# Performance work log

Hardware: AMD Instinct MI355X
Metric: run time of the kernel (lower is better)

Reference implementation:

```python
import jax, jax.numpy as jnp
import numpy as np

N = 62      # EEG channels / graph nodes
F = 5       # features per node (frequency bands)
H = 64      # num_hiddens
C = 3       # num_classes
K = 2       # SGC propagation steps
B = 32768   # batch size
BN_EPS = 1e-5
NORM_EPS = 1e-10


def setup_inputs() -> dict:
    key = jax.random.key(0)
    ks = jax.random.split(key, 8)
    n_tril = N * (N + 1) // 2  # 1953 lower-tri (incl diag) learnable edge weights
    return {
        "X": jax.random.normal(ks[0], (B, N, F), dtype=jnp.float32),
        "edge_w_tril": jax.random.normal(ks[1], (n_tril,), dtype=jnp.float32),
        "bn_gamma": jnp.ones((F,), dtype=jnp.float32),
        "bn_beta": jnp.zeros((F,), dtype=jnp.float32),
        "lin_W": jax.random.normal(ks[2], (F, H), dtype=jnp.float32) * 0.1,
        "lin_b": jax.random.normal(ks[3], (H,), dtype=jnp.float32) * 0.1,
        "fc1_W": jax.random.normal(ks[4], (N * H, 64), dtype=jnp.float32) * 0.02,
        "fc1_b": jax.random.normal(ks[5], (64,), dtype=jnp.float32) * 0.02,
        "fc2_W": jax.random.normal(ks[6], (64, C), dtype=jnp.float32) * 0.1,
        "fc2_b": jax.random.normal(ks[7], (C,), dtype=jnp.float32) * 0.1,
    }


def _propagation_matrix(edge_w_tril):
    # Rebuild symmetric learnable adjacency from lower-tri params
    xs, ys = jnp.tril_indices(N)
    W = jnp.zeros((N, N), dtype=edge_w_tril.dtype).at[xs, ys].set(edge_w_tril)
    W = W + W.T - jnp.diag(jnp.diag(W))
    # normalize_A: relu + D^{-1/2} A D^{-1/2}
    A = jax.nn.relu(W)
    d = jnp.sum(A, axis=1)
    dinv = 1.0 / jnp.sqrt(d + NORM_EPS)
    L = dinv[:, None] * A * dinv[None, :]
    # NewSGConv.norm: add self-loops (weight 1), deg = row-sum of |w|,
    # norm_ij = deg_i^{-1/2} w_ij deg_j^{-1/2}. Dense form since edge list is all-pairs.
    deg = jnp.sum(jnp.abs(L), axis=1) + 1.0  # +1 from self-loop
    dis = 1.0 / jnp.sqrt(deg)                 # deg >= 1, no inf
    S = dis[:, None] * (L + jnp.eye(N, dtype=L.dtype)) * dis[None, :]
    return S


def _forward(X, edge_w_tril, bn_gamma, bn_beta, lin_W, lin_b, fc1_W, fc1_b, fc2_W, fc2_b):
    # BatchNorm1d over feature dim (training mode: batch stats over (B, N)), biased var
    mean = jnp.mean(X, axis=(0, 1))
    var = jnp.mean(jnp.square(X - mean), axis=(0, 1))
    x = (X - mean) / jnp.sqrt(var + BN_EPS) * bn_gamma + bn_beta  # (B, N, F)

    S = _propagation_matrix(edge_w_tril)  # (N, N)
    # K steps of SGC propagation: x <- S x (gather-scale-scatter == dense matmul here)
    for _ in range(K):
        x = jnp.einsum('ij,bjf->bif', S, x)
    x = jnp.einsum('bnf,fh->bnh', x, lin_W) + lin_b  # SGConv linear, (B, N, H)

    x = x.reshape(x.shape[0], -1)                    # (B, N*H)
    x = jax.nn.relu(x @ fc1_W + fc1_b)
    return x @ fc2_W + fc2_b                         # (B, C) logits


def reference(X, edge_w_tril, bn_gamma, bn_beta, lin_W, lin_b, fc1_W, fc1_b, fc2_W, fc2_b):
    return _forward(X, edge_w_tril, bn_gamma, bn_beta, lin_W, lin_b,
                    fc1_W, fc1_b, fc2_W, fc2_b)
```

## Files before the change

kernel.cpp:

```cpp
#include <hip/hip_runtime.h>
#include <math.h>


#define STATS_BLOCKS 496
#define BN_COUNT 2031616.0f

__global__ __launch_bounds__(256) void k_stats(const float* __restrict__ X,
                                               float* __restrict__ part)
{
    int tid = blockIdx.x * 256 + threadIdx.x;
    const float4* Xv = reinterpret_cast<const float4*>(X) + (size_t)tid * 20;
    float s[5] = {0.f,0.f,0.f,0.f,0.f};
    float q[5] = {0.f,0.f,0.f,0.f,0.f};
#pragma unroll
    for (int v = 0; v < 20; ++v) {
        float4 x = Xv[v];
        s[(4*v+0)%5] += x.x; q[(4*v+0)%5] += x.x*x.x;
        s[(4*v+1)%5] += x.y; q[(4*v+1)%5] += x.y*x.y;
        s[(4*v+2)%5] += x.z; q[(4*v+2)%5] += x.z*x.z;
        s[(4*v+3)%5] += x.w; q[(4*v+3)%5] += x.w*x.w;
    }
#pragma unroll
    for (int k = 0; k < 5; ++k) {
#pragma unroll
        for (int m = 32; m >= 1; m >>= 1) {
            s[k] += __shfl_xor(s[k], m);
            q[k] += __shfl_xor(q[k], m);
        }
    }
    __shared__ float red[4][10];
    int lane = threadIdx.x & 63, w = threadIdx.x >> 6;
    if (lane == 0) {
#pragma unroll
        for (int k = 0; k < 5; ++k) { red[w][k] = s[k]; red[w][5+k] = q[k]; }
    }
    __syncthreads();
    if (threadIdx.x < 10)
        part[blockIdx.x*10 + threadIdx.x] =
            red[0][threadIdx.x] + red[1][threadIdx.x] +
            red[2][threadIdx.x] + red[3][threadIdx.x];
}

__global__ __launch_bounds__(256) void k_setup(
    const float* __restrict__ part, const float* __restrict__ edge,
    const float* __restrict__ gamma, const float* __restrict__ beta,
    const float* __restrict__ linW, const float* __restrict__ linb,
    const float* __restrict__ fc1W, const float* __restrict__ fc1b,
    float* __restrict__ Meff, float* __restrict__ constv)
{
    const int o = blockIdx.x;
    const int t = threadIdx.x;
    __shared__ float Amat[62*62];
    __shared__ float S2m[62*62];
    __shared__ float colo[3968];
    __shared__ float Tm[310];
    __shared__ float lw[320];
    __shared__ float dv[62];
    __shared__ float dis[62];
    __shared__ float scale[5], shift[5];
    __shared__ float redbuf[256];

    {
        float st[10];
#pragma unroll
        for (int k = 0; k < 10; ++k) st[k] = 0.f;
        for (int b = t; b < STATS_BLOCKS; b += 256) {
#pragma unroll
            for (int k = 0; k < 10; ++k) st[k] += part[b*10 + k];
        }
#pragma unroll
        for (int k = 0; k < 10; ++k) {
#pragma unroll
            for (int m = 32; m >= 1; m >>= 1) st[k] += __shfl_xor(st[k], m);
        }
        int lane = t & 63, w = t >> 6;
        if (lane == 0)
            for (int k = 0; k < 10; ++k) redbuf[w*10 + k] = st[k];
    }
    for (int e = t; e < 3844; e += 256) {
        int i = e / 62, j = e % 62;
        int idx = (i >= j) ? (i*(i+1)/2 + j) : (j*(j+1)/2 + i);
        Amat[e] = fmaxf(edge[idx], 0.f);
    }
    for (int i = t; i < 3968; i += 256) colo[i] = fc1W[(size_t)i*64 + o];
    for (int i = t; i < 320;  i += 256) lw[i] = linW[i];
    __syncthreads();

    if (t < 10)
        redbuf[64 + t] = redbuf[t] + redbuf[10+t] + redbuf[20+t] + redbuf[30+t];
    __syncthreads();
    if (t < 5) {
        float mean = redbuf[64 + t] * (1.0f / BN_COUNT);
        float var  = redbuf[69 + t] * (1.0f / BN_COUNT) - mean*mean;
        float inv  = 1.0f / sqrtf(var + 1e-5f);
        scale[t] = gamma[t] * inv;
        shift[t] = beta[t] - mean * gamma[t] * inv;
    }
    if (t < 62) {
        float sum = 0.f;
        for (int j = 0; j < 62; ++j) sum += Amat[t*62 + j];
        dv[t] = 1.0f / sqrtf(sum + 1e-10f);
    }
    __syncthreads();
    for (int e = t; e < 3844; e += 256) {
        int i = e / 62, j = e % 62;
        Amat[e] *= dv[i] * dv[j];
    }
    __syncthreads();
    if (t < 62) {
        float deg = 1.0f;
        for (int j = 0; j < 62; ++j) deg += fabsf(Amat[t*62 + j]);
        dis[t] = 1.0f / sqrtf(deg);
    }
    __syncthreads();
    for (int e = t; e < 3844; e += 256) {
        int i = e / 62, j = e % 62;
        float v = Amat[e] + ((i == j) ? 1.0f : 0.0f);
        Amat[e] = dis[i] * v * dis[j];
    }
    __syncthreads();
    for (int e = t; e < 3844; e += 256) {
        int i = e / 62, j = e % 62;
        float sum = 0.f;
        for (int k = 0; k < 62; ++k) sum += Amat[i*62 + k] * Amat[k*62 + j];
        S2m[e] = sum;
    }
    __syncthreads();
    for (int p = t; p < 310; p += 256) {
        int n = p / 5, f = p % 5;
        float sum = 0.f;
        for (int h = 0; h < 64; ++h) sum += lw[f*64 + h] * colo[n*64 + h];
        Tm[p] = sum;
    }
    __syncthreads();
    float cpart = 0.f;
    for (int p = t; p < 310; p += 256) {
        int j = p / 5, f = p % 5;
        float m = 0.f;
        for (int n = 0; n < 62; ++n) m += S2m[n*62 + j] * Tm[n*5 + f];
        Meff[(size_t)p*64 + o] = scale[f] * m;
        cpart += shift[f] * m;
    }
    for (int nh = t; nh < 3968; nh += 256)
        cpart += linb[nh & 63] * colo[nh];
    __syncthreads();
    redbuf[t] = cpart;
    __syncthreads();
    for (int sft = 128; sft > 0; sft >>= 1) {
        if (t < sft) redbuf[t] += redbuf[t + sft];
        __syncthreads();
    }
    if (t == 0) constv[o] = redbuf[0] + fc1b[o];
}

__global__ __launch_bounds__(256) void k_gemm(
    const float* __restrict__ X, const float* __restrict__ Meff,
    const float* __restrict__ constv, const float* __restrict__ fc2W,
    const float* __restrict__ fc2b, float* __restrict__ out)
{
    __shared__ float Ms[62*64];
    __shared__ float Xs[62*68];
    __shared__ float cst[64];
    __shared__ float f2[192];
    const int t = threadIdx.x;
    const int row0 = blockIdx.x * 64;
    const int tc = t & 15;
    const int tr = t >> 4;
    float acc[4][4];
#pragma unroll
    for (int a = 0; a < 4; ++a)
#pragma unroll
        for (int b = 0; b < 4; ++b) acc[a][b] = 0.f;

    if (t < 64)       cst[t]      = constv[t];
    else if (t < 256) { if (t - 64 < 192) f2[t - 64] = fc2W[t - 64]; }

    const int r  = t >> 2;
    const int qt = t & 3;
    const int u0 = qt * 16;
    const int ulim = (qt == 3) ? 14 : 16;

    for (int c = 0; c < 5; ++c) {
        __syncthreads();
        const float4* msrc = reinterpret_cast<const float4*>(Meff + c*3968);
        float4* mdst = reinterpret_cast<float4*>(Ms);
        for (int i = t; i < 992; i += 256) mdst[i] = msrc[i];
        const float* xrow = X + (size_t)(row0 + r)*310 + c*62 + u0;
#pragma unroll
        for (int uu = 0; uu < 16; uu += 2) {
            if (uu < ulim) {
                float2 v = *reinterpret_cast<const float2*>(xrow + uu);
                Xs[(u0 + uu    )*68 + r] = v.x;
                Xs[(u0 + uu + 1)*68 + r] = v.y;
            }
        }
        __syncthreads();
#pragma unroll 2
        for (int u = 0; u < 62; ++u) {
            float4 xv = *reinterpret_cast<const float4*>(Xs + u*68 + tr*4);
            float4 mv = *reinterpret_cast<const float4*>(Ms + u*64 + tc*4);
            acc[0][0] += xv.x*mv.x; acc[0][1] += xv.x*mv.y; acc[0][2] += xv.x*mv.z; acc[0][3] += xv.x*mv.w;
            acc[1][0] += xv.y*mv.x; acc[1][1] += xv.y*mv.y; acc[1][2] += xv.y*mv.z; acc[1][3] += xv.y*mv.w;
            acc[2][0] += xv.z*mv.x; acc[2][1] += xv.z*mv.y; acc[2][2] += xv.z*mv.z; acc[2][3] += xv.z*mv.w;
            acc[3][0] += xv.w*mv.x; acc[3][1] += xv.w*mv.y; acc[3][2] += xv.w*mv.z; acc[3][3] += xv.w*mv.w;
        }
    }

    float prt[4][3];
#pragma unroll
    for (int qq = 0; qq < 4; ++qq) { prt[qq][0] = prt[qq][1] = prt[qq][2] = 0.f; }
#pragma unroll
    for (int qq = 0; qq < 4; ++qq) {
#pragma unroll
        for (int p = 0; p < 4; ++p) {
            int col = tc*4 + p;
            float z = fmaxf(acc[qq][p] + cst[col], 0.f);
            prt[qq][0] += z * f2[col*3 + 0];
            prt[qq][1] += z * f2[col*3 + 1];
            prt[qq][2] += z * f2[col*3 + 2];
        }
    }
#pragma unroll
    for (int m = 1; m < 16; m <<= 1) {
#pragma unroll
        for (int qq = 0; qq < 4; ++qq) {
            prt[qq][0] += __shfl_xor(prt[qq][0], m);
            prt[qq][1] += __shfl_xor(prt[qq][1], m);
            prt[qq][2] += __shfl_xor(prt[qq][2], m);
        }
    }
    if (tc == 0) {
        float b0 = fc2b[0], b1 = fc2b[1], b2 = fc2b[2];
#pragma unroll
        for (int qq = 0; qq < 4; ++qq) {
            size_t rw = (size_t)(row0 + tr*4 + qq) * 3;
            out[rw + 0] = prt[qq][0] + b0;
            out[rw + 1] = prt[qq][1] + b1;
            out[rw + 2] = prt[qq][2] + b2;
        }
    }
}

extern "C" void kernel_launch(void* const* d_in, const int* in_sizes, int n_in,
                              void* d_out, int out_size, void* d_ws, size_t ws_size,
                              hipStream_t stream)
{
    const float* X     = (const float*)d_in[0];
    const float* edge  = (const float*)d_in[1];
    const float* gamma = (const float*)d_in[2];
    const float* beta  = (const float*)d_in[3];
    const float* linW  = (const float*)d_in[4];
    const float* linb  = (const float*)d_in[5];
    const float* fc1W  = (const float*)d_in[6];
    const float* fc1b  = (const float*)d_in[7];
    const float* fc2W  = (const float*)d_in[8];
    const float* fc2b  = (const float*)d_in[9];
    float* out = (float*)d_out;
    float* ws  = (float*)d_ws;

    float* part   = ws;
    float* Meff   = ws + 4960;
    float* constv = ws + 24800;

    hipLaunchKernelGGL(k_stats, dim3(496), dim3(256), 0, stream, X, part);
    hipLaunchKernelGGL(k_setup, dim3(64), dim3(256), 0, stream,
                       part, edge, gamma, beta, linW, linb, fc1W, fc1b, Meff, constv);
    hipLaunchKernelGGL(k_gemm, dim3(512), dim3(256), 0, stream,
                       X, Meff, constv, fc2W, fc2b, out);
}
```

Before: 158.4 us.

## Pre-transpose X in a separate kernel and run register-streamed GEMM without LDS

Adds a k_tp kernel that transposes X into a column-major workspace copy (XT). Its extra block computes the squared propagation matrix once instead of once per setup block. The GEMM now streams XT and Meff straight from global memory into registers with double buffering, dropping LDS staging and the per-chunk barriers, and sets launch bounds for two blocks per unit. This spends an extra full read and write of X (about 40 MB) to get coalesced vector loads and higher occupancy in the GEMM.

```diff
diff --git a/kernel.cpp b/kernel.cpp
--- a/kernel.cpp
+++ b/kernel.cpp
@@ -41,8 +41,82 @@
             red[2][threadIdx.x] + red[3][threadIdx.x];
 }
 
+__global__ __launch_bounds__(256) void k_tp(const float* __restrict__ X,
+                                            const float* __restrict__ edge,
+                                            float* __restrict__ XT,
+                                            float* __restrict__ S2g)
+{
+    __shared__ __align__(16) float lds[4160];
+    const int t = threadIdx.x;
+    if (blockIdx.x < 512) {
+        const int row0 = blockIdx.x * 64;
+        for (int cc = 0; cc < 5; ++cc) {
+            const int c0 = cc * 62;
+            if (cc) __syncthreads();
+            for (int i = t; i < 3968; i += 256) {
+                int r = i / 62, u = i - r * 62;
+                lds[u * 65 + r] = X[(size_t)(row0 + r) * 310 + c0 + u];
+            }
+            __syncthreads();
+            for (int j = t; j < 3968; j += 256) {
+                int u = j >> 6, r = j & 63;
+                XT[(size_t)(c0 + u) * 32768 + row0 + r] = lds[u * 65 + r];
+            }
+        }
+    } else {
+        float* Sm  = lds;
+        float* dv  = lds + 3968;
+        float* dis = lds + 4032;
+        for (int e = t; e < 3968; e += 256) {
+            int i = e >> 6, j = e & 63;
+            float v = 0.f;
+            if (j < 62) {
+                int idx = (i >= j) ? (i*(i+1)/2 + j) : (j*(j+1)/2 + i);
+                v = fmaxf(edge[idx], 0.f);
+            }
+            Sm[e] = v;
+        }
+        __syncthreads();
+        if (t < 62) {
+            float s = 0.f;
+            for (int j = 0; j < 64; ++j) s += Sm[t*64 + j];
+            dv[t] = 1.0f / sqrtf(s + 1e-10f);
+        }
+        __syncthreads();
+        for (int e = t; e < 3968; e += 256) {
+            int i = e >> 6, j = e & 63;
+            if (j < 62) Sm[e] *= dv[i] * dv[j];
+        }
+        __syncthreads();
+        if (t < 62) {
+            float dg = 1.0f;
+            for (int j = 0; j < 64; ++j) dg += fabsf(Sm[t*64 + j]);
+            dis[t] = 1.0f / sqrtf(dg);
+        }
+        __syncthreads();
+        for (int e = t; e < 3968; e += 256) {
+            int i = e >> 6, j = e & 63;
+            if (j < 62) {
+                float v = Sm[e] + ((i == j) ? 1.0f : 0.0f);
+                Sm[e] = dis[i] * v * dis[j];
+            }
+        }
+        __syncthreads();
+        for (int g = t; g < 992; g += 256) {
+            int i = g >> 4, j0 = (g & 15) << 2;
+            float4 acc = {0.f, 0.f, 0.f, 0.f};
+            for (int k = 0; k < 62; ++k) {
+                float s = Sm[i*64 + k];
+                float4 b = *reinterpret_cast<const float4*>(&Sm[k*64 + j0]);
+                acc.x += s*b.x; acc.y += s*b.y; acc.z += s*b.z; acc.w += s*b.w;
+            }
+            *reinterpret_cast<float4*>(&S2g[i*64 + j0]) = acc;
+        }
+    }
+}
+
 __global__ __launch_bounds__(256) void k_setup(
-    const float* __restrict__ part, const float* __restrict__ edge,
+    const float* __restrict__ part, const float* __restrict__ S2g,
     const float* __restrict__ gamma, const float* __restrict__ beta,
     const float* __restrict__ linW, const float* __restrict__ linb,
     const float* __restrict__ fc1W, const float* __restrict__ fc1b,
@@ -50,13 +124,10 @@
 {
     const int o = blockIdx.x;
     const int t = threadIdx.x;
-    __shared__ float Amat[62*62];
-    __shared__ float S2m[62*62];
+    __shared__ float S2m[3968];
     __shared__ float colo[3968];
     __shared__ float Tm[310];
     __shared__ float lw[320];
-    __shared__ float dv[62];
-    __shared__ float dis[62];
     __shared__ float scale[5], shift[5];
     __shared__ float redbuf[256];
 
@@ -77,13 +148,11 @@
         if (lane == 0)
             for (int k = 0; k < 10; ++k) redbuf[w*10 + k] = st[k];
     }
-    for (int e = t; e < 3844; e += 256) {
-        int i = e / 62, j = e % 62;
-        int idx = (i >= j) ? (i*(i+1)/2 + j) : (j*(j+1)/2 + i);
-        Amat[e] = fmaxf(edge[idx], 0.f);
-    }
-    for (int i = t; i < 3968; i += 256) colo[i] = fc1W[(size_t)i*64 + o];
-    for (int i = t; i < 320;  i += 256) lw[i] = linW[i];
+    for (int i = t; i < 3968; i += 256) {
+        S2m[i]  = S2g[i];
+        colo[i] = fc1W[(size_t)i*64 + o];
+    }
+    for (int i = t; i < 320; i += 256) lw[i] = linW[i];
     __syncthreads();
 
     if (t < 10)
@@ -96,38 +165,8 @@
         scale[t] = gamma[t] * inv;
         shift[t] = beta[t] - mean * gamma[t] * inv;
     }
-    if (t < 62) {
-        float sum = 0.f;
-        for (int j = 0; j < 62; ++j) sum += Amat[t*62 + j];
-        dv[t] = 1.0f / sqrtf(sum + 1e-10f);
-    }
-    __syncthreads();
-    for (int e = t; e < 3844; e += 256) {
-        int i = e / 62, j = e % 62;
-        Amat[e] *= dv[i] * dv[j];
-    }
-    __syncthreads();
-    if (t < 62) {
-        float deg = 1.0f;
-        for (int j = 0; j < 62; ++j) deg += fabsf(Amat[t*62 + j]);
-        dis[t] = 1.0f / sqrtf(deg);
-    }
-    __syncthreads();
-    for (int e = t; e < 3844; e += 256) {
-        int i = e / 62, j = e % 62;
-        float v = Amat[e] + ((i == j) ? 1.0f : 0.0f);
-        Amat[e] = dis[i] * v * dis[j];
-    }
-    __syncthreads();
-    for (int e = t; e < 3844; e += 256) {
-        int i = e / 62, j = e % 62;
-        float sum = 0.f;
-        for (int k = 0; k < 62; ++k) sum += Amat[i*62 + k] * Amat[k*62 + j];
-        S2m[e] = sum;
-    }
-    __syncthreads();
     for (int p = t; p < 310; p += 256) {
-        int n = p / 5, f = p % 5;
+        int n = p / 5, f = p - n*5;
         float sum = 0.f;
         for (int h = 0; h < 64; ++h) sum += lw[f*64 + h] * colo[n*64 + h];
         Tm[p] = sum;
@@ -135,9 +174,9 @@
     __syncthreads();
     float cpart = 0.f;
     for (int p = t; p < 310; p += 256) {
-        int j = p / 5, f = p % 5;
+        int j = p / 5, f = p - j*5;
         float m = 0.f;
-        for (int n = 0; n < 62; ++n) m += S2m[n*62 + j] * Tm[n*5 + f];
+        for (int n = 0; n < 62; ++n) m += S2m[n*64 + j] * Tm[n*5 + f];
         Meff[(size_t)p*64 + o] = scale[f] * m;
         cpart += shift[f] * m;
     }
@@ -153,90 +192,97 @@
     if (t == 0) constv[o] = redbuf[0] + fc1b[o];
 }
 
-__global__ __launch_bounds__(256) void k_gemm(
-    const float* __restrict__ X, const float* __restrict__ Meff,
+struct Ch { float4 xa[5]; float4 m[5]; };
+
+__device__ __forceinline__ void ldch(Ch& c, const float* px, const float* pm, int u0) {
+#pragma unroll
+    for (int k = 0; k < 5; ++k) {
+        c.xa[k] = *reinterpret_cast<const float4*>(px + (size_t)(u0 + k) * 32768);
+        c.m[k]  = *reinterpret_cast<const float4*>(pm + (u0 + k) * 64);
+    }
+}
+
+__device__ __forceinline__ void fmach(float acc[4][4], const Ch& c) {
+#pragma unroll
+    for (int k = 0; k < 5; ++k) {
+        float4 x = c.xa[k], m = c.m[k];
+        acc[0][0] += x.x*m.x; acc[0][1] += x.x*m.y; acc[0][2] += x.x*m.z; acc[0][3] += x.x*m.w;
+        acc[1][0] += x.y*m.x; acc[1][1] += x.y*m.y; acc[1][2] += x.y*m.z; acc[1][3] += x.y*m.w;
+        acc[2][0] += x.z*m.x; acc[2][1] += x.z*m.y; acc[2][2] += x.z*m.z; acc[2][3] += x.z*m.w;
+        acc[3][0] += x.w*m.x; acc[3][1] += x.w*m.y; acc[3][2] += x.w*m.z; acc[3][3] += x.w*m.w;
+    }
+}
+
+__global__ __launch_bounds__(256, 2) void k_gemm(
+    const float* __restrict__ XT, const float* __restrict__ Meff,
     const float* __restrict__ constv, const float* __restrict__ fc2W,
     const float* __restrict__ fc2b, float* __restrict__ out)
 {
-    __shared__ float Ms[62*64];
-    __shared__ float Xs[62*68];
-    __shared__ float cst[64];
-    __shared__ float f2[192];
     const int t = threadIdx.x;
-    const int row0 = blockIdx.x * 64;
     const int tc = t & 15;
     const int tr = t >> 4;
+    const int row0 = blockIdx.x * 64;
+    const float* px = XT + row0 + tr * 4;
+    const float* pm = Meff + tc * 4;
     float acc[4][4];
 #pragma unroll
     for (int a = 0; a < 4; ++a)
 #pragma unroll
         for (int b = 0; b < 4; ++b) acc[a][b] = 0.f;
 
-    if (t < 64)       cst[t]      = constv[t];
-    else if (t < 256) { if (t - 64 < 192) f2[t - 64] = fc2W[t - 64]; }
-
-    const int r  = t >> 2;
-    const int qt = t & 3;
-    const int u0 = qt * 16;
-    const int ulim = (qt == 3) ? 14 : 16;
-
-    for (int c = 0; c < 5; ++c) {
-        __syncthreads();
-        const float4* msrc = reinterpret_cast<const float4*>(Meff + c*3968);
-        float4* mdst = reinterpret_cast<float4*>(Ms);
-        for (int i = t; i < 992; i += 256) mdst[i] = msrc[i];
-        const float* xrow = X + (size_t)(row0 + r)*310 + c*62 + u0;
-#pragma unroll
-        for (int uu = 0; uu < 16; uu += 2) {
-            if (uu < ulim) {
-                float2 v = *reinterpret_cast<const float2*>(xrow + uu);
-                Xs[(u0 + uu    )*68 + r] = v.x;
-                Xs[(u0 + uu + 1)*68 + r] = v.y;
-            }
-        }
-        __syncthreads();
-#pragma unroll 2
-        for (int u = 0; u < 62; ++u) {
-            float4 xv = *reinterpret_cast<const float4*>(Xs + u*68 + tr*4);
-            float4 mv = *reinterpret_cast<const float4*>(Ms + u*64 + tc*4);
-            acc[0][0] += xv.x*mv.x; acc[0][1] += xv.x*mv.y; acc[0][2] += xv.x*mv.z; acc[0][3] += xv.x*mv.w;
-            acc[1][0] += xv.y*mv.x; acc[1][1] += xv.y*mv.y; acc[1][2] += xv.y*mv.z; acc[1][3] += xv.y*mv.w;
-            acc[2][0] += xv.z*mv.x; acc[2][1] += xv.z*mv.y; acc[2][2] += xv.z*mv.z; acc[2][3] += xv.z*mv.w;
-            acc[3][0] += xv.w*mv.x; acc[3][1] += xv.w*mv.y; acc[3][2] += xv.w*mv.z; acc[3][3] += xv.w*mv.w;
-        }
-    }
-
+    Ch A, B;
+    ldch(A, px, pm, 0);
+#pragma unroll 1
+    for (int i = 0; i < 30; ++i) {
+        ldch(B, px, pm, 5);
+        fmach(acc, A);
+        px += 10 * 32768; pm += 10 * 64;
+        ldch(A, px, pm, 0);
+        fmach(acc, B);
+    }
+    ldch(B, px, pm, 5);
+    fmach(acc, A);
+    fmach(acc, B);
+
+    float cst[4], f2r[4][3];
+#pragma unroll
+    for (int j = 0; j < 4; ++j) {
+        int col = tc*4 + j;
+        cst[j]    = constv[col];
+        f2r[j][0] = fc2W[col*3 + 0];
+        f2r[j][1] = fc2W[col*3 + 1];
+        f2r[j][2] = fc2W[col*3 + 2];
+    }
     float prt[4][3];
 #pragma unroll
-    for (int qq = 0; qq < 4; ++qq) { prt[qq][0] = prt[qq][1] = prt[qq][2] = 0.f; }
-#pragma unroll
-    for (int qq = 0; qq < 4; ++qq) {
-#pragma unroll
-        for (int p = 0; p < 4; ++p) {
-            int col = tc*4 + p;
-            float z = fmaxf(acc[qq][p] + cst[col], 0.f);
-            prt[qq][0] += z * f2[col*3 + 0];
-            prt[qq][1] += z * f2[col*3 + 1];
-            prt[qq][2] += z * f2[col*3 + 2];
+    for (int q = 0; q < 4; ++q) { prt[q][0] = prt[q][1] = prt[q][2] = 0.f; }
+#pragma unroll
+    for (int q = 0; q < 4; ++q) {
+#pragma unroll
+        for (int j = 0; j < 4; ++j) {
+            float z = fmaxf(acc[q][j] + cst[j], 0.f);
+            prt[q][0] += z * f2r[j][0];
+            prt[q][1] += z * f2r[j][1];
+            prt[q][2] += z * f2r[j][2];
         }
     }
 #pragma unroll
     for (int m = 1; m < 16; m <<= 1) {
 #pragma unroll
-        for (int qq = 0; qq < 4; ++qq) {
-            prt[qq][0] += __shfl_xor(prt[qq][0], m);
-            prt[qq][1] += __shfl_xor(prt[qq][1], m);
-            prt[qq][2] += __shfl_xor(prt[qq][2], m);
+        for (int q = 0; q < 4; ++q) {
+            prt[q][0] += __shfl_xor(prt[q][0], m);
+            prt[q][1] += __shfl_xor(prt[q][1], m);
+            prt[q][2] += __shfl_xor(prt[q][2], m);
         }
     }
     if (tc == 0) {
         float b0 = fc2b[0], b1 = fc2b[1], b2 = fc2b[2];
 #pragma unroll
-        for (int qq = 0; qq < 4; ++qq) {
-            size_t rw = (size_t)(row0 + tr*4 + qq) * 3;
-            out[rw + 0] = prt[qq][0] + b0;
-            out[rw + 1] = prt[qq][1] + b1;
-            out[rw + 2] = prt[qq][2] + b2;
+        for (int q = 0; q < 4; ++q) {
+            size_t rw = (size_t)(row0 + tr*4 + q) * 3;
+            out[rw + 0] = prt[q][0] + b0;
+            out[rw + 1] = prt[q][1] + b1;
+            out[rw + 2] = prt[q][2] + b2;
         }
     }
 }
@@ -259,12 +305,15 @@
     float* ws  = (float*)d_ws;
 
     float* part   = ws;
-    float* Meff   = ws + 4960;
-    float* constv = ws + 24800;
+    float* S2g    = ws + 4960;
+    float* Meff   = ws + 8928;
+    float* constv = ws + 28768;
+    float* XT     = ws + 32768;
 
     hipLaunchKernelGGL(k_stats, dim3(496), dim3(256), 0, stream, X, part);
-    hipLaunchKernelGGL(k_setup, dim3(64), dim3(256), 0, stream,
-                       part, edge, gamma, beta, linW, linb, fc1W, fc1b, Meff, constv);
-    hipLaunchKernelGGL(k_gemm, dim3(512), dim3(256), 0, stream,
-                       X, Meff, constv, fc2W, fc2b, out);
-}
+    hipLaunchKernelGGL(k_tp,    dim3(513), dim3(256), 0, stream, X, edge, XT, S2g);
+    hipLaunchKernelGGL(k_setup, dim3(64),  dim3(256), 0, stream,
+                       part, S2g, gamma, beta, linW, linb, fc1W, fc1b, Meff, constv);
+    hipLaunchKernelGGL(k_gemm,  dim3(512), dim3(256), 0, stream,
+                       XT, Meff, constv, fc2W, fc2b, out);
+}
```

Result: slower. 168.1 us (+6.1%).
